# Kernel optimization log

Measured on AMD Instinct MI355X. Metric: run time of the kernel, lower is better.

Reference implementation:

```python
import jax, jax.numpy as jnp
import numpy as np

LN_EPS = 1e-5

def layer_norm(x, w, b):
    mu = jnp.mean(x, axis=-1, keepdims=True)
    var = jnp.mean(jnp.square(x - mu), axis=-1, keepdims=True)
    return (x - mu) * jax.lax.rsqrt(var + LN_EPS) * w + b

def adaptive_mask_np(aa, bb, ada_para=0.2):
    # True = disallowed (matches torch ~bool mask). Static shapes -> numpy.
    adaptive_num = int(bb * ada_para)
    cc = bb // aa
    i = np.arange(aa)
    start = i * cc
    end = start + cc + adaptive_num
    over = end > bb - 1
    start = np.where(over, np.maximum(start - (end - (bb - 1)), 0), start)
    end = np.where(over, bb, end)
    cols = np.arange(bb)
    allowed = (cols[None, :] >= start[:, None]) & (cols[None, :] < end[:, None])
    return jnp.asarray(~allowed)  # [aa, bb] bool

def setup_inputs() -> dict:
    key = jax.random.key(0)
    ks = jax.random.split(key, 20)
    Lq, Lk, B, d, dff = 512, 4096, 4, 512, 2048
    s = lambda k, shape: jax.random.normal(k, shape, dtype=jnp.float32) * 0.02
    inp = {
        'tgt': jax.random.normal(ks[0], (Lq, B, d), dtype=jnp.float32),
        'memory': jax.random.normal(ks[1], (Lk, B, d), dtype=jnp.float32),
        'Wq': s(ks[2], (d, d)), 'bq': jnp.zeros((d,), jnp.float32),
        'Wk': s(ks[3], (d, d)), 'bk': jnp.zeros((d,), jnp.float32),
        'Wv': s(ks[4], (d, d)), 'bv': jnp.zeros((d,), jnp.float32),
        'Wo': s(ks[5], (d, d)), 'bo': jnp.zeros((d,), jnp.float32),
        'W1': s(ks[6], (dff, d)), 'b1': jnp.zeros((dff,), jnp.float32),
        'W2': s(ks[7], (d, dff)), 'b2': jnp.zeros((d,), jnp.float32),
        'ln1_w': jnp.ones((d,), jnp.float32), 'ln1_b': jnp.zeros((d,), jnp.float32),
        'ln2_w': jnp.ones((d,), jnp.float32), 'ln2_b': jnp.zeros((d,), jnp.float32),
        'ln3_w': jnp.ones((d,), jnp.float32), 'ln3_b': jnp.zeros((d,), jnp.float32),
        'ln4_w': jnp.ones((d,), jnp.float32), 'ln4_b': jnp.zeros((d,), jnp.float32),
    }
    return inp

def reference(tgt, memory, Wq, bq, Wk, bk, Wv, bv, Wo, bo, W1, b1, W2, b2,
              ln1_w, ln1_b, ln2_w, ln2_b, ln3_w, ln3_b, ln4_w, ln4_b):
    Lq, B, d = tgt.shape
    Lk = memory.shape[0]
    H = 8
    hd = d // H
    scale = 1.0 / jnp.sqrt(jnp.asarray(hd, tgt.dtype))

    t = layer_norm(tgt, ln1_w, ln1_b)      # [Lq,B,d]
    m = layer_norm(memory, ln2_w, ln2_b)   # [Lk,B,d]

    mask = adaptive_mask_np(Lq, Lk, 0.2)   # [Lq,Lk] bool, True=masked

    q = (t @ Wq.T + bq).reshape(Lq, B, H, hd)
    k = (m @ Wk.T + bk).reshape(Lk, B, H, hd)
    v = (m @ Wv.T + bv).reshape(Lk, B, H, hd)

    scores = jnp.einsum('qbhd,kbhd->bhqk', q * scale, k)
    scores = jnp.where(mask[None, None], -jnp.inf, scores)
    p = jax.nn.softmax(scores, axis=-1)                   # [B,H,Lq,Lk]
    attn_weights = jnp.mean(p, axis=1)                    # [B,Lq,Lk] (avg over heads)

    ctx = jnp.einsum('bhqk,kbhd->qbhd', p, v).reshape(Lq, B, d)
    tgt2 = ctx @ Wo.T + bo

    x = t + tgt2                       # dropout1 = identity (eval)
    x = layer_norm(x, ln3_w, ln3_b)
    ff = jax.nn.relu(x @ W1.T + b1) @ W2.T + b2
    x = x + ff                         # dropout2 = identity (eval)
    x = layer_norm(x, ln4_w, ln4_b)
    return (x, attn_weights)
```

## Files before the change

kernel.cpp:

```cpp
#include <hip/hip_runtime.h>
#include <hip/hip_bf16.h>

typedef __hip_bfloat16 bf16_t;
typedef __bf16 bf16x8 __attribute__((ext_vector_type(8)));
typedef float f32x4 __attribute__((ext_vector_type(4)));

#define LQ 512
#define LK 4096
#define BATCH 4
#define DMODEL 512
#define NHEAD 8
#define HEADDIM 64
#define DFF 2048
#define LN_EPS 1e-5f

#define KSTR 2064
#define VSTR 4112

__device__ inline float tofl(float x) { return x; }
__device__ inline float tofl(bf16_t x) { return __bfloat162float(x); }
__device__ inline void stfl(float* p, float v) { *p = v; }
__device__ inline void stfl(bf16_t* p, float v) { *p = __float2bfloat16(v); }

__device__ __forceinline__ void gld_lds16(const bf16_t* g, void* lds_base) {
    __builtin_amdgcn_global_load_lds(
        (const __attribute__((address_space(1))) uint32_t*)g,
        (__attribute__((address_space(3))) uint32_t*)lds_base, 16, 0, 0);
}

__global__ void prep_kernel(const float* __restrict__ s0, const float* __restrict__ s1,
                            const float* __restrict__ s2, const float* __restrict__ s3,
                            const float* __restrict__ s4,
                            bf16_t* __restrict__ wqkvo, bf16_t* __restrict__ w1bf,
                            float* __restrict__ zbuf) {
    int bid = blockIdx.x;
    int tid = threadIdx.x;
    if (bid < 2048) {
        int t = bid * 256 + tid;
        int which = t >> 16;
        int idx = (t & 65535) * 4;
        const float* s; bf16_t* d;
        if (which < 4) {
            s = (which == 0 ? s0 : which == 1 ? s1 : which == 2 ? s2 : s3);
            d = wqkvo + (size_t)which * 262144;
        } else {
            s = s4 + (size_t)(which - 4) * 262144;
            d = w1bf + (size_t)(which - 4) * 262144;
        }
        float4 v = *(const float4*)(s + idx);
        d[idx + 0] = __float2bfloat16(v.x);
        d[idx + 1] = __float2bfloat16(v.y);
        d[idx + 2] = __float2bfloat16(v.z);
        d[idx + 3] = __float2bfloat16(v.w);
    } else {
        size_t i = ((size_t)(bid - 2048) * 256 + tid) * 4;
        float4 z = {0.f, 0.f, 0.f, 0.f};
        *(float4*)(zbuf + i) = z;
    }
}

__global__ void conv_w2(const float* __restrict__ s, bf16_t* __restrict__ d) {
    int i = (blockIdx.x * 256 + threadIdx.x) * 4;
    float4 v = *(const float4*)(s + i);
    d[i + 0] = __float2bfloat16(v.x);
    d[i + 1] = __float2bfloat16(v.y);
    d[i + 2] = __float2bfloat16(v.z);
    d[i + 3] = __float2bfloat16(v.w);
}

template <typename TOUT, bool DUAL>
__global__ void ln_kernel(const float* __restrict__ in, const float* __restrict__ w,
                          const float* __restrict__ b, TOUT* __restrict__ out1,
                          float* __restrict__ out2) {
    __shared__ float red[256];
    const int row = blockIdx.x;
    const int tid = threadIdx.x;
    const float* x = in + (size_t)row * DMODEL;
    float v0 = x[tid];
    float v1 = x[tid + 256];

    red[tid] = v0 + v1;
    __syncthreads();
    for (int s = 128; s > 0; s >>= 1) { if (tid < s) red[tid] += red[tid + s]; __syncthreads(); }
    float mu = red[0] * (1.0f / DMODEL);
    __syncthreads();

    float d0 = v0 - mu, d1 = v1 - mu;
    red[tid] = d0 * d0 + d1 * d1;
    __syncthreads();
    for (int s = 128; s > 0; s >>= 1) { if (tid < s) red[tid] += red[tid + s]; __syncthreads(); }
    float inv = rsqrtf(red[0] * (1.0f / DMODEL) + LN_EPS);

    float r0 = d0 * inv * w[tid] + b[tid];
    float r1 = d1 * inv * w[tid + 256] + b[tid + 256];
    TOUT* o = out1 + (size_t)row * DMODEL;
    stfl(&o[tid], r0);
    stfl(&o[tid + 256], r1);
    if (DUAL) {
        float* o2 = out2 + (size_t)row * DMODEL;
        o2[tid] = r0;
        o2[tid + 256] = r1;
    }
}

__global__ void ln12_kernel(const float* __restrict__ tgt, const float* __restrict__ memory,
                            const float* __restrict__ w1, const float* __restrict__ b1,
                            const float* __restrict__ w2, const float* __restrict__ b2,
                            bf16_t* __restrict__ t_bf, float* __restrict__ t_f32,
                            bf16_t* __restrict__ m_buf) {
    __shared__ float red[256];
    const int row = blockIdx.x;
    const int tid = threadIdx.x;
    const float* in; const float* w; const float* b;
    bf16_t* o1; float* o2; bool dual;
    if (row < 2048) {
        in = tgt + (size_t)row * DMODEL; w = w1; b = b1;
        o1 = t_bf + (size_t)row * DMODEL; o2 = t_f32 + (size_t)row * DMODEL; dual = true;
    } else {
        int r2 = row - 2048;
        in = memory + (size_t)r2 * DMODEL; w = w2; b = b2;
        o1 = m_buf + (size_t)r2 * DMODEL; o2 = nullptr; dual = false;
    }
    float v0 = in[tid];
    float v1 = in[tid + 256];
    red[tid] = v0 + v1;
    __syncthreads();
    for (int s = 128; s > 0; s >>= 1) { if (tid < s) red[tid] += red[tid + s]; __syncthreads(); }
    float mu = red[0] * (1.0f / DMODEL);
    __syncthreads();
    float d0 = v0 - mu, d1 = v1 - mu;
    red[tid] = d0 * d0 + d1 * d1;
    __syncthreads();
    for (int s = 128; s > 0; s >>= 1) { if (tid < s) red[tid] += red[tid + s]; __syncthreads(); }
    float inv = rsqrtf(red[0] * (1.0f / DMODEL) + LN_EPS);
    float r0 = d0 * inv * w[tid] + b[tid];
    float r1 = d1 * inv * w[tid + 256] + b[tid + 256];
    o1[tid] = __float2bfloat16(r0);
    o1[tid + 256] = __float2bfloat16(r1);
    if (dual) {
        o2[tid] = r0;
        o2[tid + 256] = r1;
    }
}

template <int TN, typename TC, bool RELU, bool RESID, bool KREMAP = false>
__global__ __launch_bounds__(256) void gemm_mfma(
        const bf16_t* __restrict__ A, const bf16_t* __restrict__ B,
        const float* __restrict__ bias, const float* __restrict__ resid,
        TC* __restrict__ C, int M, int N, int K) {
    __shared__ uint4 As4[1024];
    __shared__ uint4 Bs4[TN * 8];

    const int tid = threadIdx.x;
    const int lane = tid & 63;
    const int wave = tid >> 6;
    const int row16 = lane & 15;
    const int quad = lane >> 4;
    const int n0 = blockIdx.x * TN;
    const int m0 = blockIdx.y * 128;

    constexpr int MI = (TN == 128) ? 4 : 2;
    const int wy = (TN == 128) ? (wave >> 1) : wave;
    const int wx = (TN == 128) ? (wave & 1) : 0;
    const int m_base = wy * ((TN == 128) ? 64 : 32);
    const int n_base = wx * 64;

    const int rr = lane >> 3;
    const int kc = (lane & 7) ^ rr;
    const int kx = row16 & 7;

    const bf16_t* AsE = (const bf16_t*)As4;
    const bf16_t* BsE = (const bf16_t*)Bs4;

    f32x4 acc[MI][4] = {};

    for (int k0 = 0; k0 < K; k0 += 64) {
#pragma unroll
        for (int it = 0; it < 4; it++) {
            int issue = it * 4 + wave;
            int r = issue * 8 + rr;
            gld_lds16(A + (size_t)(m0 + r) * K + k0 + kc * 8, &As4[issue * 64]);
        }
#pragma unroll
        for (int it = 0; it < TN / 32; it++) {
            int issue = it * 4 + wave;
            int r = issue * 8 + rr;
            gld_lds16(B + (size_t)(n0 + r) * K + k0 + kc * 8, &Bs4[issue * 64]);
        }
        __syncthreads();
#pragma unroll
        for (int s = 0; s < 2; s++) {
            const int kq = s * 4 + quad;
            const int kcs = (kq ^ kx) * 8;
            bf16x8 af[MI], bfr[4];
#pragma unroll
            for (int i = 0; i < MI; i++)
                af[i] = *(const bf16x8*)&AsE[(m_base + i * 16 + row16) * 64 + kcs];
#pragma unroll
            for (int j = 0; j < 4; j++)
                bfr[j] = *(const bf16x8*)&BsE[(n_base + j * 16 + row16) * 64 + kcs];
#pragma unroll
            for (int i = 0; i < MI; i++)
#pragma unroll
                for (int j = 0; j < 4; j++)
                    acc[i][j] = __builtin_amdgcn_mfma_f32_16x16x32_bf16(af[i], bfr[j], acc[i][j], 0, 0, 0);
        }
        __syncthreads();
    }

#pragma unroll
    for (int i = 0; i < MI; i++) {
#pragma unroll
        for (int j = 0; j < 4; j++) {
            int col = n0 + n_base + j * 16 + row16;
            float bsv = bias[col];
#pragma unroll
            for (int r = 0; r < 4; r++) {
                int row = m0 + m_base + i * 16 + quad * 4 + r;
                float val = acc[i][j][r] + bsv;
                if (RESID) val += resid[(size_t)row * N + col];
                if (RELU) val = fmaxf(val, 0.0f);
                size_t caddr = KREMAP
                    ? ((size_t)(row >> 2) * KSTR + (size_t)(row & 3) * 512 + col)
                    : ((size_t)row * N + col);
                stfl(&C[caddr], val);
            }
        }
    }
}

__global__ __launch_bounds__(256) void transpose_kv(const bf16_t* __restrict__ kb,
                                                    bf16_t* __restrict__ kT) {
    __shared__ bf16_t tile[64][80];
    const int kt = blockIdx.x * 64;
    const int ct = blockIdx.y * 64;
    const int b  = blockIdx.z;
    const int t = threadIdx.x;
    {
        int kl = t >> 2, cl = (t & 3) * 16;
        const bf16_t* src = kb + ((size_t)(kt + kl) * 4 + b) * 512 + ct + cl;
        *(uint4*)&tile[kl][cl]     = *(const uint4*)src;
        *(uint4*)&tile[kl][cl + 8] = *(const uint4*)(src + 8);
    }
    __syncthreads();
    {
        int cl2 = t >> 2, ks = (t & 3) * 16;
        __attribute__((aligned(16))) bf16_t vals[16];
#pragma unroll
        for (int j = 0; j < 16; j++) vals[j] = tile[ks + j][cl2];
        bf16_t* dst = kT + ((size_t)b * 512 + ct + cl2) * VSTR + kt + ks;
        *(uint4*)dst       = *(const uint4*)&vals[0];
        *(uint4*)(dst + 8) = *(const uint4*)&vals[8];
    }
}

__global__ __launch_bounds__(512, 1) void attn_mfma(
        const bf16_t* __restrict__ qb,
        const bf16_t* __restrict__ kb,
        const bf16_t* __restrict__ vT,
        bf16_t* __restrict__ ctx,
        float* __restrict__ attn_out) {
    extern __shared__ char smem[];
    bf16_t* Ps   = (bf16_t*)smem;
    bf16_t* Qs   = (bf16_t*)(smem + 115712);
    bf16_t* Zrow = (bf16_t*)(smem + 115712 + 8320);
    float*  Ls   = (float*)(smem + 115712 + 8320 + 1808);

    const int b  = blockIdx.x & 3;
    const int qt = blockIdx.x >> 2;
    const int q0 = qt * 8;
    const int tid = threadIdx.x;
    const int lane = tid & 63;
    const int h = tid >> 6;
    const int hoffg = h * HEADDIM;
    const int row16 = lane & 15;
    const int quad = lane >> 4;

    int us; { int s = q0 * 8, e = s + 827; if (e > 4095) s = 3268; us = s; }
    int sq[4], eq[4];
#pragma unroll
    for (int r = 0; r < 4; r++) {
        int ql = quad * 4 + r;
        if (ql < 8) {
            int s = (q0 + ql) * 8, e = s + 827;
            if (e > 4095) { s = 3268; e = 4096; }
            sq[r] = s; eq[r] = e;
        } else { sq[r] = 0; eq[r] = 0; }
    }

    {
        int r = tid >> 6, coff = (tid & 63) * 8;
        *(uint4*)&Qs[r * 520 + coff] =
            *(const uint4*)(qb + ((size_t)(q0 + r) * 4 + b) * 512 + coff);
        if (tid < 113) { uint4 z = {0, 0, 0, 0}; *(uint4*)&Zrow[tid * 8] = z; }
    }
    __syncthreads();

    const bf16_t* q0p = (row16 < 8) ? &Qs[row16 * 520 + hoffg + quad * 8] : &Zrow[0];
    const bf16_t* q1p = (row16 < 8) ? &Qs[row16 * 520 + hoffg + 32 + quad * 8] : &Zrow[8];
    const bf16x8 aq0 = *(const bf16x8*)q0p;
    const bf16x8 aq1 = *(const bf16x8*)q1p;

    float l[4] = {0.f, 0.f, 0.f, 0.f};
#pragma unroll 4
    for (int it = 0; it < 56; ++it) {
        int key = us + it * 16 + row16;
        int key_eff = key > 4095 ? 4095 : key;
        const bf16_t* kr = kb + (size_t)key_eff * KSTR + b * 512 + hoffg;
        bf16x8 bk0 = *(const bf16x8*)(kr + quad * 8);
        bf16x8 bk1 = *(const bf16x8*)(kr + 32 + quad * 8);
        f32x4 acc = {};
        acc = __builtin_amdgcn_mfma_f32_16x16x32_bf16(aq0, bk0, acc, 0, 0, 0);
        acc = __builtin_amdgcn_mfma_f32_16x16x32_bf16(aq1, bk1, acc, 0, 0, 0);
#pragma unroll
        for (int r = 0; r < 4; r++) {
            int ql = quad * 4 + r;
            bool valid = (key >= sq[r]) && (key < eq[r]);
            float p = valid ? __expf(0.125f * acc[r]) : 0.0f;
            l[r] += p;
            if (ql < 8) Ps[(h * 8 + ql) * 904 + it * 16 + row16] = __float2bfloat16(p);
        }
    }
#pragma unroll
    for (int off = 1; off < 16; off <<= 1) {
#pragma unroll
        for (int r = 0; r < 4; r++) l[r] += __shfl_xor(l[r], off, 64);
    }
    float linv[4];
#pragma unroll
    for (int r = 0; r < 4; r++) linv[r] = 1.0f / l[r];
    if (row16 == 0) {
#pragma unroll
        for (int r = 0; r < 4; r++) {
            int ql = quad * 4 + r;
            if (ql < 8) Ls[h * 8 + ql] = linv[r];
        }
    }
    __syncthreads();

    f32x4 o[4] = {};
#pragma unroll 2
    for (int it = 0; it < 28; ++it) {
        const bf16_t* ap_src = (row16 < 8) ? &Ps[(h * 8 + row16) * 904 + it * 32 + quad * 8]
                                           : &Zrow[0];
        bf16x8 ap = *(const bf16x8*)ap_src;
#pragma unroll
        for (int nt = 0; nt < 4; ++nt) {
            const bf16_t* vr = vT + ((size_t)(b * 512 + hoffg + nt * 16 + row16)) * VSTR
                               + us + it * 32 + quad * 8;
            bf16x8 bv = *(const bf16x8*)vr;
            o[nt] = __builtin_amdgcn_mfma_f32_16x16x32_bf16(ap, bv, o[nt], 0, 0, 0);
        }
    }

    {
        int qq = h;
        float ls[8];
#pragma unroll
        for (int hh = 0; hh < 8; ++hh) ls[hh] = 0.125f * Ls[hh * 8 + qq];
        float* base = attn_out + ((size_t)b * LQ + q0 + qq) * LK + us;
        const int cmax = LK - us;
        for (int col = lane; col < 896; col += 64) {
            if (col < cmax) {
                float s = 0.f;
#pragma unroll
                for (int hh = 0; hh < 8; ++hh) s += ls[hh] * tofl(Ps[(hh * 8 + qq) * 904 + col]);
                base[col] = s;
            }
        }
    }

#pragma unroll
    for (int nt = 0; nt < 4; nt++) {
#pragma unroll
        for (int r = 0; r < 4; r++) {
            int ql = quad * 4 + r;
            if (ql < 8) {
                ctx[((size_t)(q0 + ql) * 4 + b) * 512 + hoffg + nt * 16 + row16] =
                    __float2bfloat16(o[nt][r] * linv[r]);
            }
        }
    }
}

extern "C" void kernel_launch(void* const* d_in, const int* in_sizes, int n_in,
                              void* d_out, int out_size, void* d_ws, size_t ws_size,
                              hipStream_t stream) {
    const float* tgt    = (const float*)d_in[0];
    const float* memory = (const float*)d_in[1];
    const float* Wq = (const float*)d_in[2];
    const float* bq = (const float*)d_in[3];
    const float* Wk = (const float*)d_in[4];
    const float* bk = (const float*)d_in[5];
    const float* Wv = (const float*)d_in[6];
    const float* bv = (const float*)d_in[7];
    const float* Wo = (const float*)d_in[8];
    const float* bo = (const float*)d_in[9];
    const float* W1 = (const float*)d_in[10];
    const float* b1 = (const float*)d_in[11];
    const float* W2 = (const float*)d_in[12];
    const float* b2 = (const float*)d_in[13];
    const float* ln1w = (const float*)d_in[14];
    const float* ln1b = (const float*)d_in[15];
    const float* ln2w = (const float*)d_in[16];
    const float* ln2b = (const float*)d_in[17];
    const float* ln3w = (const float*)d_in[18];
    const float* ln3b = (const float*)d_in[19];
    const float* ln4w = (const float*)d_in[20];
    const float* ln4b = (const float*)d_in[21];

    const size_t M1 = (size_t)LQ * BATCH;
    const size_t M2 = (size_t)LK * BATCH;
    const size_t SZ1 = M1 * DMODEL;

    char* wsb = (char*)d_ws;
    const size_t MB = 1 << 20;
    bf16_t* m_buf   = (bf16_t*)(wsb + 0 * MB);
    bf16_t* vT_buf  = (bf16_t*)(wsb + 0 * MB);
    bf16_t* h_buf   = (bf16_t*)(wsb + 0 * MB);
    bf16_t* k_buf   = (bf16_t*)(wsb + 17 * MB);
    float*  xres    = (float*)(wsb + 17 * MB);
    float*  xln_f   = (float*)(wsb + 21 * MB);
    float*  x2_buf  = (float*)(wsb + 25 * MB);
    bf16_t* W2_bf   = (bf16_t*)(wsb + 34 * MB);
    bf16_t* v_buf   = (bf16_t*)(wsb + 34 * MB);
    bf16_t* t_bf    = (bf16_t*)(wsb + 50 * MB);
    bf16_t* xln_bf  = (bf16_t*)(wsb + 50 * MB);
    float*  t_f32   = (float*)(wsb + 52 * MB);
    bf16_t* q_bf    = (bf16_t*)(wsb + 56 * MB);
    bf16_t* ctx_buf = (bf16_t*)(wsb + 58 * MB);
    bf16_t* wqkvo   = (bf16_t*)(wsb + 60 * MB);
    bf16_t* W1_bf   = (bf16_t*)(wsb + 62 * MB);

    bf16_t* Wq_bf = wqkvo;
    bf16_t* Wk_bf = wqkvo + 262144;
    bf16_t* Wv_bf = wqkvo + 2 * 262144;
    bf16_t* Wo_bf = wqkvo + 3 * 262144;

    float* out_x    = (float*)d_out;
    float* out_attn = out_x + SZ1;

    prep_kernel<<<dim3(10240), dim3(256), 0, stream>>>(
        Wq, Wk, Wv, Wo, W1, wqkvo, W1_bf, out_attn);

    ln12_kernel<<<dim3(M1 + M2), dim3(256), 0, stream>>>(
        tgt, memory, ln1w, ln1b, ln2w, ln2b, t_bf, t_f32, m_buf);

    gemm_mfma<64, bf16_t, false, false><<<dim3(8, 16), dim3(256), 0, stream>>>(
        t_bf, Wq_bf, bq, nullptr, q_bf, M1, DMODEL, DMODEL);
    gemm_mfma<128, bf16_t, false, false, true><<<dim3(4, 128), dim3(256), 0, stream>>>(
        m_buf, Wk_bf, bk, nullptr, k_buf, M2, DMODEL, DMODEL);
    gemm_mfma<128, bf16_t, false, false><<<dim3(4, 128), dim3(256), 0, stream>>>(
        m_buf, Wv_bf, bv, nullptr, v_buf, M2, DMODEL, DMODEL);

    transpose_kv<<<dim3(64, 8, 4), dim3(256), 0, stream>>>(v_buf, vT_buf);

    conv_w2<<<dim3(1024), dim3(256), 0, stream>>>(W2, W2_bf);

    const int attn_lds = 115712 + 8320 + 1808 + 256;
    hipFuncSetAttribute((const void*)attn_mfma,
                        hipFuncAttributeMaxDynamicSharedMemorySize, attn_lds);
    attn_mfma<<<dim3(256), dim3(512), attn_lds, stream>>>(
        q_bf, k_buf, vT_buf, ctx_buf, out_attn);

    gemm_mfma<64, float, false, true><<<dim3(8, 16), dim3(256), 0, stream>>>(
        ctx_buf, Wo_bf, bo, t_f32, xres, M1, DMODEL, DMODEL);

    ln_kernel<bf16_t, true><<<dim3(M1), dim3(256), 0, stream>>>(xres, ln3w, ln3b, xln_bf, xln_f);

    gemm_mfma<128, bf16_t, true, false><<<dim3(16, 16), dim3(256), 0, stream>>>(
        xln_bf, W1_bf, b1, nullptr, h_buf, M1, DFF, DMODEL);

    gemm_mfma<64, float, false, true><<<dim3(8, 16), dim3(256), 0, stream>>>(
        h_buf, W2_bf, b2, xln_f, x2_buf, M1, DMODEL, DFF);

    ln_kernel<float, false><<<dim3(M1), dim3(256), 0, stream>>>(x2_buf, ln4w, ln4b, out_x, nullptr);
}
```

Measured before the change: 325.1 us.

## Write full attn rows with zeros in-kernel, drop separate zero-fill pass, pad K/V strides

The attention kernel now writes each full 4096-wide row of averaged attention weights using float4 stores, emitting zeros outside the allowed window. This removes the zero-fill of the 32 MB attn output that prep_kernel used to do, so that buffer is written once instead of twice. Block-to-(batch, query tile) mapping is reordered so neighbouring blocks share a batch and adjacent query tiles, and the K/V row strides are padded further, likely to reduce cache or channel conflicts. The cost is extra per-lane branching and more store instructions inside attention.

```diff
diff --git a/kernel.cpp b/kernel.cpp
--- a/kernel.cpp
+++ b/kernel.cpp
@@ -14,8 +14,8 @@
 #define DFF 2048
 #define LN_EPS 1e-5f
 
-#define KSTR 2064
-#define VSTR 4112
+#define KSTR 2080
+#define VSTR 4128
 
 __device__ inline float tofl(float x) { return x; }
 __device__ inline float tofl(bf16_t x) { return __bfloat162float(x); }
@@ -31,32 +31,23 @@
 __global__ void prep_kernel(const float* __restrict__ s0, const float* __restrict__ s1,
                             const float* __restrict__ s2, const float* __restrict__ s3,
                             const float* __restrict__ s4,
-                            bf16_t* __restrict__ wqkvo, bf16_t* __restrict__ w1bf,
-                            float* __restrict__ zbuf) {
-    int bid = blockIdx.x;
-    int tid = threadIdx.x;
-    if (bid < 2048) {
-        int t = bid * 256 + tid;
-        int which = t >> 16;
-        int idx = (t & 65535) * 4;
-        const float* s; bf16_t* d;
-        if (which < 4) {
-            s = (which == 0 ? s0 : which == 1 ? s1 : which == 2 ? s2 : s3);
-            d = wqkvo + (size_t)which * 262144;
-        } else {
-            s = s4 + (size_t)(which - 4) * 262144;
-            d = w1bf + (size_t)(which - 4) * 262144;
-        }
-        float4 v = *(const float4*)(s + idx);
-        d[idx + 0] = __float2bfloat16(v.x);
-        d[idx + 1] = __float2bfloat16(v.y);
-        d[idx + 2] = __float2bfloat16(v.z);
-        d[idx + 3] = __float2bfloat16(v.w);
+                            bf16_t* __restrict__ wqkvo, bf16_t* __restrict__ w1bf) {
+    int t = blockIdx.x * 256 + threadIdx.x;
+    int which = t >> 16;
+    int idx = (t & 65535) * 4;
+    const float* s; bf16_t* d;
+    if (which < 4) {
+        s = (which == 0 ? s0 : which == 1 ? s1 : which == 2 ? s2 : s3);
+        d = wqkvo + (size_t)which * 262144;
     } else {
-        size_t i = ((size_t)(bid - 2048) * 256 + tid) * 4;
-        float4 z = {0.f, 0.f, 0.f, 0.f};
-        *(float4*)(zbuf + i) = z;
-    }
+        s = s4 + (size_t)(which - 4) * 262144;
+        d = w1bf + (size_t)(which - 4) * 262144;
+    }
+    float4 v = *(const float4*)(s + idx);
+    d[idx + 0] = __float2bfloat16(v.x);
+    d[idx + 1] = __float2bfloat16(v.y);
+    d[idx + 2] = __float2bfloat16(v.z);
+    d[idx + 3] = __float2bfloat16(v.w);
 }
 
 __global__ void conv_w2(const float* __restrict__ s, bf16_t* __restrict__ d) {
@@ -266,8 +257,9 @@
     bf16_t* Zrow = (bf16_t*)(smem + 115712 + 8320);
     float*  Ls   = (float*)(smem + 115712 + 8320 + 1808);
 
-    const int b  = blockIdx.x & 3;
-    const int qt = blockIdx.x >> 2;
+    const int blk = blockIdx.x;
+    const int b  = (blk & 7) >> 1;
+    const int qt = ((blk >> 3) << 1) | (blk & 1);
     const int q0 = qt * 8;
     const int tid = threadIdx.x;
     const int lane = tid & 63;
@@ -358,15 +350,26 @@
         float ls[8];
 #pragma unroll
         for (int hh = 0; hh < 8; ++hh) ls[hh] = 0.125f * Ls[hh * 8 + qq];
-        float* base = attn_out + ((size_t)b * LQ + q0 + qq) * LK + us;
-        const int cmax = LK - us;
-        for (int col = lane; col < 896; col += 64) {
-            if (col < cmax) {
-                float s = 0.f;
-#pragma unroll
-                for (int hh = 0; hh < 8; ++hh) s += ls[hh] * tofl(Ps[(hh * 8 + qq) * 904 + col]);
-                base[col] = s;
+        float* rowp = attn_out + ((size_t)b * LQ + q0 + qq) * LK;
+        const bf16_t* ps = Ps + qq * 904;
+        for (int it = 0; it < 16; ++it) {
+            int c4 = (it * 64 + lane) * 4;
+            float4 v = {0.f, 0.f, 0.f, 0.f};
+            int off = c4 - us;
+            if (off >= -3 && off < 896) {
+#pragma unroll
+                for (int e = 0; e < 4; ++e) {
+                    int pc = off + e;
+                    float s = 0.f;
+                    if (pc >= 0 && pc < 896) {
+#pragma unroll
+                        for (int hh = 0; hh < 8; ++hh)
+                            s += ls[hh] * tofl(ps[hh * 8 * 904 + pc]);
+                    }
+                    (&v.x)[e] = s;
+                }
             }
+            *(float4*)(rowp + c4) = v;
         }
     }
 
@@ -440,8 +443,8 @@
     float* out_x    = (float*)d_out;
     float* out_attn = out_x + SZ1;
 
-    prep_kernel<<<dim3(10240), dim3(256), 0, stream>>>(
-        Wq, Wk, Wv, Wo, W1, wqkvo, W1_bf, out_attn);
+    prep_kernel<<<dim3(2048), dim3(256), 0, stream>>>(
+        Wq, Wk, Wv, Wo, W1, wqkvo, W1_bf);
 
     ln12_kernel<<<dim3(M1 + M2), dim3(256), 0, stream>>>(
         tgt, memory, ln1w, ln1b, ln2w, ln2b, t_bf, t_f32, m_buf);
```

Result: faster. 317.6 us (-2.3%).
